# Kernel tuning notes

Measured on AMD Instinct MI355X. Metric: run time of the kernel, lower is better.

The kernel has to match this reference:

```python
import jax, jax.numpy as jnp
import numpy as np

B, S, T = 128, 1024, 512
VOCAB, E, HE, HD, ATT = 1000, 128, 64, 66, 32


def setup_inputs() -> dict:
    key = jax.random.key(0)
    ks = jax.random.split(key, 14)
    p = lambda k, shape: (jax.random.normal(k, shape, dtype=jnp.float32) * 0.05)
    return {
        'x': jax.random.randint(ks[0], (B, S), 0, VOCAB, dtype=jnp.int32),
        'c': jax.random.normal(ks[1], (B, T), dtype=jnp.float32),
        'emb': p(ks[2], (VOCAB, E)),
        'enc_Wih': p(ks[3], (4 * HE, E)),
        'enc_Whh': p(ks[4], (4 * HE, HE)),
        'enc_b': p(ks[5], (4 * HE,)),
        'att_fc_W': p(ks[6], (HE, E)),
        'att_fc_b': p(ks[7], (HE,)),
        'att_w_W': p(ks[8], (ATT, HE)),
        'att_w_b': p(ks[9], (ATT,)),
        'dec_Wih': p(ks[10], (4 * HD, ATT)),
        'dec_Whh': p(ks[11], (4 * HD, HD)),
        'dec_b': p(ks[12], (4 * HD,)),
        'fin_W': p(ks[13], (E, HD)),
        'fin_b': jnp.zeros((E,), dtype=jnp.float32),
    }


def _lstm_seq(xs, W_ih, W_hh, b, H):
    # xs: [B, S, in]; PyTorch gate order i, f, g, o
    bsz = xs.shape[0]
    gx = jnp.einsum('bsi,gi->bsg', xs, W_ih) + b  # [B,S,4H]

    def step(carry, g_t):
        h, c = carry
        g = g_t + h @ W_hh.T
        i, f, gg, o = jnp.split(g, 4, axis=-1)
        c = jax.nn.sigmoid(f) * c + jax.nn.sigmoid(i) * jnp.tanh(gg)
        h = jax.nn.sigmoid(o) * jnp.tanh(c)
        return (h, c), h

    h0 = jnp.zeros((bsz, H), xs.dtype)
    (_, _), hs = jax.lax.scan(step, (h0, h0), jnp.swapaxes(gx, 0, 1))
    return jnp.swapaxes(hs, 0, 1)  # [B,S,H]


def reference(x, c, emb, enc_Wih, enc_Whh, enc_b, att_fc_W, att_fc_b,
              att_w_W, att_w_b, dec_Wih, dec_Whh, dec_b, fin_W, fin_b):
    # encoder: embed + LSTM, returns full sequence of hidden states [B,S,64]
    enc = _lstm_seq(emb[x], enc_Wih, enc_Whh, enc_b, HE)
    bsz, steps = x.shape[0], c.shape[1]
    # initial decoder input: embedding of token 0, broadcast over batch
    x0 = jnp.broadcast_to(emb[0], (bsz, E))
    h0 = jnp.zeros((bsz, HD), enc.dtype)

    def step(carry, _):
        xemb, h, cc = carry
        # attend(a=xemb, A=enc)
        a = xemb @ att_fc_W.T + att_fc_b                     # [B,64]
        A = a[:, None, :] * enc                              # [B,S,64]
        alpha = jax.nn.softmax(
            jnp.tanh(jnp.einsum('bse,ae->bsa', A, att_w_W) + att_w_b),
            axis=-1)                                         # [B,S,32]
        beta = alpha.sum(axis=1)                             # [B,32]
        # decoder LSTM cell (one timestep)
        g = beta @ dec_Wih.T + h @ dec_Whh.T + dec_b
        i, f, gg, o = jnp.split(g, 4, axis=-1)
        cc = jax.nn.sigmoid(f) * cc + jax.nn.sigmoid(i) * jnp.tanh(gg)
        h = jax.nn.sigmoid(o) * jnp.tanh(cc)
        xemb = h @ fin_W.T + fin_b                           # feed back via final_fc
        return (xemb, h, cc), h

    _, hs = jax.lax.scan(step, (x0, h0, h0), None, length=steps)
    return jnp.swapaxes(hs, 0, 1)  # [B,T,66]
```

## Files before the change

kernel.cpp:

```cpp
#include <hip/hip_runtime.h>
#include <hip/hip_bf16.h>

#define kB 128
#define kS 1024
#define kT 512
#define kV 1000
#define kE 128
#define kHE 64
#define kHD 66
#define kATT 32
#define kGE 256
#define kGD 264

typedef __attribute__((ext_vector_type(4))) float f32x4;
typedef __attribute__((ext_vector_type(8))) short bf16x8;
typedef __attribute__((ext_vector_type(8))) unsigned short u16x8;

__device__ __forceinline__ unsigned short f2bf(float f) {
  unsigned int u = __builtin_bit_cast(unsigned int, f);
  u += 0x7FFFu + ((u >> 16) & 1u);
  return (unsigned short)(u >> 16);
}
__device__ __forceinline__ float rcp_(float x) { return __builtin_amdgcn_rcpf(x); }
__device__ __forceinline__ float fsig(float x)  { return rcp_(1.0f + __expf(-x)); }
__device__ __forceinline__ float ftanh(float x) { return 1.0f - 2.0f * rcp_(1.0f + __expf(2.0f * x)); }
__device__ __forceinline__ float fexp2(float z) {
#if __has_builtin(__builtin_amdgcn_exp2f)
  return __builtin_amdgcn_exp2f(z);
#else
  return __expf(z * 0.6931471805599453f);
#endif
}
__device__ __forceinline__ const unsigned short* launder_us(const unsigned short* p) {
  asm volatile("" : "+s"(p));
  return p;
}
__device__ __forceinline__ float dpp_red16(float v) {
  int x = __builtin_bit_cast(int, v);
  v += __builtin_bit_cast(float, __builtin_amdgcn_update_dpp(0, x, 0xB1, 0xf, 0xf, true));
  x = __builtin_bit_cast(int, v);
  v += __builtin_bit_cast(float, __builtin_amdgcn_update_dpp(0, x, 0x4E, 0xf, 0xf, true));
  x = __builtin_bit_cast(int, v);
  v += __builtin_bit_cast(float, __builtin_amdgcn_update_dpp(0, x, 0x124, 0xf, 0xf, true));
  x = __builtin_bit_cast(int, v);
  v += __builtin_bit_cast(float, __builtin_amdgcn_update_dpp(0, x, 0x128, 0xf, 0xf, true));
  return v;
}

__global__ __launch_bounds__(256) void prep_kernel(
    const float* __restrict__ emb, const float* __restrict__ enc_Wih,
    const float* __restrict__ enc_b, const float* __restrict__ enc_Whh,
    const float* __restrict__ att_fc_W, const float* __restrict__ att_fc_b,
    const float* __restrict__ att_w_W,
    const float* __restrict__ fin_W, const float* __restrict__ fin_b,
    const float* __restrict__ dec_Wih, const float* __restrict__ dec_Whh,
    const float* __restrict__ dec_b,
    float* __restrict__ embW, unsigned short* __restrict__ decF,
    unsigned short* __restrict__ encF, unsigned short* __restrict__ afF,
    float* __restrict__ wregF, float* __restrict__ dbias,
    float* __restrict__ wh64, float* __restrict__ wh65,
    float* __restrict__ abias, float* __restrict__ ainit) {
  int bid = blockIdx.x, tid = threadIdx.x;
  if (bid < kV) {
    float acc = enc_b[tid];
    const float* er = emb + bid * kE;
    const float* wr = enc_Wih + tid * kE;
    for (int e = 0; e < kE; ++e) acc += er[e] * wr[e];
    embW[bid * kGE + tid] = acc;
  } else if (bid == kV) {
    for (int i = tid; i < 17 * 3 * 64 * 8; i += 256) {
      int jj = i & 7, lane = (i >> 3) & 63, ts = i >> 9;
      int tile = ts / 3, ks = ts - tile * 3;
      int j = tile * 16 + (lane & 15);
      int k = ks * 32 + ((lane >> 4) << 3) + jj;
      float v = 0.f;
      if (j < kGD) {
        if (k < 32) v = dec_Wih[j * kATT + k];
        else v = dec_Whh[j * kHD + (k - 32)];
      }
      decF[i] = f2bf(v);
    }
  } else if (bid == kV + 1) {
    for (int i = tid; i < 16 * 2 * 64 * 8; i += 256) {
      int jj = i & 7, lane = (i >> 3) & 63, ts = i >> 9;
      int tile = ts >> 1, ks = ts & 1;
      int j = tile * 16 + (lane & 15);
      int k = ks * 32 + ((lane >> 4) << 3) + jj;
      encF[i] = f2bf(enc_Whh[j * kHE + k]);
    }
  } else if (bid == kV + 2) {
    for (int i = tid; i < 4 * 3 * 64 * 8; i += 256) {
      int jj = i & 7, lane = (i >> 3) & 63, ts = i >> 9;
      int tile = ts / 3, ks = ts - tile * 3;
      int aidx = tile * 16 + (lane & 15);
      int m = ks * 32 + ((lane >> 4) << 3) + jj;
      float v = 0.f;
      if (m < kHD)
        for (int e = 0; e < kE; ++e) v += att_fc_W[aidx * kE + e] * fin_W[e * kHD + m];
      afF[i] = f2bf(v);
    }
  } else if (bid == kV + 3) {
    for (int i = tid; i < 8 * 64 * 4; i += 256) {
      int c = i & 3, lane = (i >> 2) & 63, jq = i >> 8;
      int half = jq & 1, kc = (jq >> 1) & 1, mt = jq >> 2;
      wregF[i] = att_w_W[(mt * 16 + (lane & 15)) * kHE + kc * 32 + ((lane >> 4) << 3) + half * 4 + c];
    }
  } else if (bid == kV + 4) {
    for (int j = tid; j < kGD; j += 256) {
      float s = 0.f;
      for (int m = 0; m < kATT; ++m) s += dec_Wih[j * kATT + m];
      dbias[j] = dec_b[j] + 32.0f * s;
      wh64[j] = dec_Whh[j * kHD + 64];
      wh65[j] = dec_Whh[j * kHD + 65];
    }
  } else {
    if (tid < kHE) {
      float acc = att_fc_b[tid];
      for (int e = 0; e < kE; ++e) acc += att_fc_W[tid * kE + e] * fin_b[e];
      abias[tid] = acc;
    } else if (tid < 2 * kHE) {
      int a = tid - kHE;
      float acc = att_fc_b[a];
      for (int e = 0; e < kE; ++e) acc += emb[e] * att_fc_W[a * kE + e];
      ainit[a] = acc;
    }
  }
}

__global__ __launch_bounds__(256)
__attribute__((amdgpu_waves_per_eu(1, 1)))
void enc_kernel(
    const int* __restrict__ x, const float* __restrict__ embW,
    const unsigned short* __restrict__ encF, float* __restrict__ out) {
  __shared__ struct __align__(16) {
    unsigned short xe[64];
    float gbuf[kGE];
    int toks[kS];
  } sm;
  const int b = blockIdx.x, t = threadIdx.x, lane = t & 63, wv = t >> 6;

  for (int i = t; i < kS; i += 256) sm.toks[i] = x[b * kS + i];
  if (t < 64) sm.xe[t] = 0;

  u16x8 eQ[4][2];
  #pragma unroll
  for (int q = 0; q < 4; ++q)
    #pragma unroll
    for (int ks = 0; ks < 2; ++ks)
      eQ[q][ks] = *(const u16x8*)&encF[(((wv * 4 + q) * 2 + ks) * 64 + lane) * 8];
  __syncthreads();

  float gx0 = 0, gx1 = 0, gx2 = 0, gx3 = 0;
  if (lane < 16) {
    int tok = sm.toks[0];
    gx0 = embW[tok * kGE + wv * 64 + 0 + lane];
    gx1 = embW[tok * kGE + wv * 64 + 16 + lane];
    gx2 = embW[tok * kGE + wv * 64 + 32 + lane];
    gx3 = embW[tok * kGE + wv * 64 + 48 + lane];
  }
  float cE = 0.0f;
  unsigned short* eg = (unsigned short*)(out + (size_t)b * (kT * kHD));

  for (int s = 0; s < kS; ++s) {
    union { u16x8 u; bf16x8 v; } xa0, xa1;
    xa0.u = *(const u16x8*)&sm.xe[(lane >> 4) << 3];
    xa1.u = *(const u16x8*)&sm.xe[32 + ((lane >> 4) << 3)];
    float gn0 = 0, gn1 = 0, gn2 = 0, gn3 = 0;
    int tokn = sm.toks[(s + 1 < kS) ? (s + 1) : s];
    if (lane < 16) {
      gn0 = embW[tokn * kGE + wv * 64 + 0 + lane];
      gn1 = embW[tokn * kGE + wv * 64 + 16 + lane];
      gn2 = embW[tokn * kGE + wv * 64 + 32 + lane];
      gn3 = embW[tokn * kGE + wv * 64 + 48 + lane];
    }
    f32x4 z = {0.f, 0.f, 0.f, 0.f};
    f32x4 a0 = __builtin_amdgcn_mfma_f32_16x16x32_bf16(xa0.v, eQ[0][0], z, 0, 0, 0);
    a0 = __builtin_amdgcn_mfma_f32_16x16x32_bf16(xa1.v, eQ[0][1], a0, 0, 0, 0);
    f32x4 a1 = __builtin_amdgcn_mfma_f32_16x16x32_bf16(xa0.v, eQ[1][0], z, 0, 0, 0);
    a1 = __builtin_amdgcn_mfma_f32_16x16x32_bf16(xa1.v, eQ[1][1], a1, 0, 0, 0);
    f32x4 a2 = __builtin_amdgcn_mfma_f32_16x16x32_bf16(xa0.v, eQ[2][0], z, 0, 0, 0);
    a2 = __builtin_amdgcn_mfma_f32_16x16x32_bf16(xa1.v, eQ[2][1], a2, 0, 0, 0);
    f32x4 a3 = __builtin_amdgcn_mfma_f32_16x16x32_bf16(xa0.v, eQ[3][0], z, 0, 0, 0);
    a3 = __builtin_amdgcn_mfma_f32_16x16x32_bf16(xa1.v, eQ[3][1], a3, 0, 0, 0);
    if (lane < 16) {
      sm.gbuf[wv * 64 + 0 + lane]  = a0[0] + gx0;
      sm.gbuf[wv * 64 + 16 + lane] = a1[0] + gx1;
      sm.gbuf[wv * 64 + 32 + lane] = a2[0] + gx2;
      sm.gbuf[wv * 64 + 48 + lane] = a3[0] + gx3;
    }
    __syncthreads();
    if (t < 64) {
      float gi = sm.gbuf[t], gf = sm.gbuf[64 + t], gg = sm.gbuf[128 + t], go = sm.gbuf[192 + t];
      cE = fsig(gf) * cE + fsig(gi) * ftanh(gg);
      float h = fsig(go) * ftanh(cE);
      unsigned short hb = f2bf(h);
      sm.xe[t] = hb;
      eg[s * 64 + ((((t >> 3) ^ (s & 7)) << 3) | (t & 7))] = hb;
    }
    __syncthreads();
    gx0 = gn0; gx1 = gn1; gx2 = gn2; gx3 = gn3;
  }
}

struct __align__(16) DSm {
  unsigned short enc[kS * kHE];
  float wregL[8 * 64 * 4];
  unsigned short afL[4 * 3 * 64 * 8];
  float dbL[kGD];
  float wh64L[kGD];
  float wh65L[kGD];
  float absL[64];
  float aa[64];
  float beta[32];
  unsigned short xv[160];
  float gbuf[kGD];
  float hh2[2];
};

union U8 { u16x8 u; bf16x8 v; };

__global__ __launch_bounds__(512, 2)
void dec_kernel(
    const float* __restrict__ att_w_b,
    const unsigned short* __restrict__ decF, const unsigned short* __restrict__ afF,
    const float* __restrict__ wregF_ws, const float* __restrict__ dbias_ws,
    const float* __restrict__ wh64_ws, const float* __restrict__ wh65_ws,
    const float* __restrict__ abias_ws, const float* __restrict__ ainit_ws,
    float* __restrict__ out) {
  __shared__ DSm sm;
  const int b = blockIdx.x, t = threadIdx.x, lane = t & 63, wv = t >> 6;
  const int lr = lane & 15, g = lane >> 4;

  {
    const u16x8* src = (const u16x8*)(out + (size_t)b * (kT * kHD));
    u16x8* dst = (u16x8*)sm.enc;
    #pragma unroll
    for (int i = 0; i < 16; ++i) dst[t + i * 512] = src[t + i * 512];
  }
  ((f32x4*)sm.wregL)[t] = ((const f32x4*)wregF_ws)[t];
  for (int i = t; i < 768; i += 512) ((u16x8*)sm.afL)[i] = ((const u16x8*)afF)[i];
  for (int i = t; i < kGD; i += 512) {
    sm.dbL[i] = dbias_ws[i];
    sm.wh64L[i] = wh64_ws[i];
    sm.wh65L[i] = wh65_ws[i];
  }
  if (t < 64) { sm.absL[t] = abias_ws[t]; sm.aa[t] = ainit_ws[t]; }
  if (t < 32) sm.beta[t] = 0.f;
  if (t < 160) sm.xv[t] = 0;
  if (t < 2) sm.hh2[t] = 0.f;

  f32x4 wb0, wb1;
  #pragma unroll
  for (int r = 0; r < 4; ++r) {
    wb0[r] = att_w_b[g * 4 + r];
    wb1[r] = att_w_b[16 + g * 4 + r];
  }
  float cD = 0.0f, cD2 = 0.0f;
  __syncthreads();

  const int sbase = wv * 128;
  const int tileA = wv, tileB = wv + 8;
  const bool has3 = (wv == 7);

  for (int step = 0; step < kT; ++step) {
    U8 qa[3], qb[3], qc[3];
    {
      const f32x4* aap = (const f32x4*)sm.aa;
      const f32x4* wrl = (const f32x4*)sm.wregL;
      bf16x8 af[2][2];
      #pragma unroll
      for (int kc = 0; kc < 2; ++kc) {
        f32x4 a0v = aap[kc * 8 + g * 2];
        f32x4 a1v = aap[kc * 8 + g * 2 + 1];
        #pragma unroll
        for (int mt = 0; mt < 2; ++mt) {
          f32x4 w0 = wrl[((mt * 2 + kc) * 2 + 0) * 64 + lane];
          f32x4 w1 = wrl[((mt * 2 + kc) * 2 + 1) * 64 + lane];
          union { bf16x8 v; __hip_bfloat162 h2[4]; } tmp;
          tmp.h2[0] = __float22bfloat162_rn(make_float2(w0.x * a0v.x, w0.y * a0v.y));
          tmp.h2[1] = __float22bfloat162_rn(make_float2(w0.z * a0v.z, w0.w * a0v.w));
          tmp.h2[2] = __float22bfloat162_rn(make_float2(w1.x * a1v.x, w1.y * a1v.y));
          tmp.h2[3] = __float22bfloat162_rn(make_float2(w1.z * a1v.z, w1.w * a1v.w));
          af[mt][kc] = tmp.v;
        }
      }
      float betaAcc[2][4] = {};
      float amax = 0.0f;
      #pragma unroll
      for (int nt = 0; nt < 8; ++nt) {
        int s = sbase + nt * 16 + lr;
        int sw = s & 7;
        U8 e0, e1;
        e0.u = *(const u16x8*)&sm.enc[s * kHE + ((g ^ sw) << 3)];
        e1.u = *(const u16x8*)&sm.enc[s * kHE + (((4 + g) ^ sw) << 3)];
        f32x4 acc0 = __builtin_amdgcn_mfma_f32_16x16x32_bf16(af[0][0], e0.v, wb0, 0, 0, 0);
        acc0 = __builtin_amdgcn_mfma_f32_16x16x32_bf16(af[0][1], e1.v, acc0, 0, 0, 0);
        f32x4 acc1 = __builtin_amdgcn_mfma_f32_16x16x32_bf16(af[1][0], e0.v, wb1, 0, 0, 0);
        acc1 = __builtin_amdgcn_mfma_f32_16x16x32_bf16(af[1][1], e1.v, acc1, 0, 0, 0);
        float u0[4], u1[4], dsum = 0.f;
        #pragma unroll
        for (int r = 0; r < 4; ++r) {
          float x0 = acc0[r], x1 = acc1[r];
          amax = fmaxf(amax, fmaxf(__builtin_fabsf(x0), __builtin_fabsf(x1)));
          u0[r] = fexp2(x0 * __builtin_fmaf(x0 * x0, -0.48089835f, 1.44269504f));
          u1[r] = fexp2(x1 * __builtin_fmaf(x1 * x1, -0.48089835f, 1.44269504f));
          dsum += u0[r] + u1[r];
        }
        dsum += __shfl_xor(dsum, 16);
        dsum += __shfl_xor(dsum, 32);
        float invd = rcp_(dsum);
        #pragma unroll
        for (int r = 0; r < 4; ++r) {
          betaAcc[0][r] += u0[r] * invd;
          betaAcc[1][r] += u1[r] * invd;
        }
      }
      if (__builtin_expect(__any(amax > 0.35f), 0)) {
        #pragma unroll
        for (int mt = 0; mt < 2; ++mt)
          #pragma unroll
          for (int r = 0; r < 4; ++r) betaAcc[mt][r] = 0.f;
        for (int nt = 0; nt < 8; ++nt) {
          int s = sbase + nt * 16 + lr;
          int sw = s & 7;
          U8 e0, e1;
          e0.u = *(const u16x8*)&sm.enc[s * kHE + ((g ^ sw) << 3)];
          e1.u = *(const u16x8*)&sm.enc[s * kHE + (((4 + g) ^ sw) << 3)];
          f32x4 acc0 = __builtin_amdgcn_mfma_f32_16x16x32_bf16(af[0][0], e0.v, wb0, 0, 0, 0);
          acc0 = __builtin_amdgcn_mfma_f32_16x16x32_bf16(af[0][1], e1.v, acc0, 0, 0, 0);
          f32x4 acc1 = __builtin_amdgcn_mfma_f32_16x16x32_bf16(af[1][0], e0.v, wb1, 0, 0, 0);
          acc1 = __builtin_amdgcn_mfma_f32_16x16x32_bf16(af[1][1], e1.v, acc1, 0, 0, 0);
          float u0[4], u1[4], dsum = 0.f;
          for (int r = 0; r < 4; ++r) {
            u0[r] = __expf(tanhf(acc0[r]));
            u1[r] = __expf(tanhf(acc1[r]));
            dsum += u0[r] + u1[r];
          }
          dsum += __shfl_xor(dsum, 16);
          dsum += __shfl_xor(dsum, 32);
          float invd = rcp_(dsum);
          for (int r = 0; r < 4; ++r) {
            betaAcc[0][r] += u0[r] * invd;
            betaAcc[1][r] += u1[r] * invd;
          }
        }
      }
      {
        const unsigned short* dFp = launder_us(decF);
        #pragma unroll
        for (int ks = 0; ks < 3; ++ks) {
          qa[ks].u = *(const u16x8*)&dFp[((tileA * 3 + ks) * 64 + lane) * 8];
          qb[ks].u = *(const u16x8*)&dFp[((tileB * 3 + ks) * 64 + lane) * 8];
        }
        if (has3) {
          #pragma unroll
          for (int ks = 0; ks < 3; ++ks)
            qc[ks].u = *(const u16x8*)&dFp[((16 * 3 + ks) * 64 + lane) * 8];
        }
      }
      #pragma unroll
      for (int mt = 0; mt < 2; ++mt)
        #pragma unroll
        for (int r = 0; r < 4; ++r) {
          float v = dpp_red16(betaAcc[mt][r]);
          if (lr == 0) atomicAdd(&sm.beta[mt * 16 + g * 4 + r], v);
        }
    }
    __syncthreads();
    {
      const f32x4* pb = (const f32x4*)sm.beta;
      f32x4 b0 = pb[g * 2], b1 = pb[g * 2 + 1];
      union { bf16x8 v; __hip_bfloat162 h2[4]; } bfr;
      bfr.h2[0] = __float22bfloat162_rn(make_float2(b0.x - 32.f, b0.y - 32.f));
      bfr.h2[1] = __float22bfloat162_rn(make_float2(b0.z - 32.f, b0.w - 32.f));
      bfr.h2[2] = __float22bfloat162_rn(make_float2(b1.x - 32.f, b1.y - 32.f));
      bfr.h2[3] = __float22bfloat162_rn(make_float2(b1.z - 32.f, b1.w - 32.f));
      U8 xg1, xg2;
      xg1.u = *(const u16x8*)&sm.xv[32 + (g << 3)];
      xg2.u = *(const u16x8*)&sm.xv[64 + (g << 3)];
      float hh0 = sm.hh2[0], hh1 = sm.hh2[1];
      f32x4 z = {0.f, 0.f, 0.f, 0.f};
      f32x4 ga = __builtin_amdgcn_mfma_f32_16x16x32_bf16(bfr.v, qa[0].v, z, 0, 0, 0);
      ga = __builtin_amdgcn_mfma_f32_16x16x32_bf16(xg1.v, qa[1].v, ga, 0, 0, 0);
      ga = __builtin_amdgcn_mfma_f32_16x16x32_bf16(xg2.v, qa[2].v, ga, 0, 0, 0);
      f32x4 gb = __builtin_amdgcn_mfma_f32_16x16x32_bf16(bfr.v, qb[0].v, z, 0, 0, 0);
      gb = __builtin_amdgcn_mfma_f32_16x16x32_bf16(xg1.v, qb[1].v, gb, 0, 0, 0);
      gb = __builtin_amdgcn_mfma_f32_16x16x32_bf16(xg2.v, qb[2].v, gb, 0, 0, 0);
      if (lane < 16) {
        int ja = tileA * 16 + lane;
        sm.gbuf[ja] = ga[0] + sm.dbL[ja] + sm.wh64L[ja] * hh0 + sm.wh65L[ja] * hh1;
        int jb = tileB * 16 + lane;
        sm.gbuf[jb] = gb[0] + sm.dbL[jb] + sm.wh64L[jb] * hh0 + sm.wh65L[jb] * hh1;
      }
      if (has3) {
        f32x4 gc = __builtin_amdgcn_mfma_f32_16x16x32_bf16(bfr.v, qc[0].v, z, 0, 0, 0);
        gc = __builtin_amdgcn_mfma_f32_16x16x32_bf16(xg1.v, qc[1].v, gc, 0, 0, 0);
        gc = __builtin_amdgcn_mfma_f32_16x16x32_bf16(xg2.v, qc[2].v, gc, 0, 0, 0);
        if (lane < 8) {
          int jc = 256 + lane;
          sm.gbuf[jc] = gc[0] + sm.dbL[jc] + sm.wh64L[jc] * hh0 + sm.wh65L[jc] * hh1;
        }
      }
    }
    __syncthreads();
    if (wv == 0) {
      float gi = sm.gbuf[lane], gf = sm.gbuf[66 + lane], gg = sm.gbuf[132 + lane], go = sm.gbuf[198 + lane];
      cD = fsig(gf) * cD + fsig(gi) * ftanh(gg);
      float h = fsig(go) * ftanh(cD);
      sm.xv[32 + lane] = f2bf(h);
      out[((size_t)b * kT + step) * kHD + lane] = h;
      if (lane < 2) {
        float gi2 = sm.gbuf[64 + lane], gf2 = sm.gbuf[130 + lane], gg2 = sm.gbuf[196 + lane], go2 = sm.gbuf[262 + lane];
        cD2 = fsig(gf2) * cD2 + fsig(gi2) * ftanh(gg2);
        float h2 = fsig(go2) * ftanh(cD2);
        sm.xv[96 + lane] = f2bf(h2);
        sm.hh2[lane] = h2;
        out[((size_t)b * kT + step) * kHD + 64 + lane] = h2;
      }
      U8 y0, y1, y2;
      y0.u = *(const u16x8*)&sm.xv[32 + (g << 3)];
      y1.u = *(const u16x8*)&sm.xv[64 + (g << 3)];
      y2.u = *(const u16x8*)&sm.xv[96 + (g << 3)];
      f32x4 z = {0.f, 0.f, 0.f, 0.f};
      #pragma unroll
      for (int tt = 0; tt < 4; ++tt) {
        U8 f0, f1, f2;
        f0.u = *(const u16x8*)&sm.afL[((tt * 3 + 0) * 64 + lane) * 8];
        f1.u = *(const u16x8*)&sm.afL[((tt * 3 + 1) * 64 + lane) * 8];
        f2.u = *(const u16x8*)&sm.afL[((tt * 3 + 2) * 64 + lane) * 8];
        f32x4 acc = __builtin_amdgcn_mfma_f32_16x16x32_bf16(y0.v, f0.v, z, 0, 0, 0);
        acc = __builtin_amdgcn_mfma_f32_16x16x32_bf16(y1.v, f1.v, acc, 0, 0, 0);
        acc = __builtin_amdgcn_mfma_f32_16x16x32_bf16(y2.v, f2.v, acc, 0, 0, 0);
        if (lane < 16) sm.aa[tt * 16 + lane] = acc[0] + sm.absL[tt * 16 + lane];
      }
      if (lane < 32) sm.beta[lane] = 0.f;
    }
    __syncthreads();
  }
}

extern "C" void kernel_launch(void* const* d_in, const int* in_sizes, int n_in,
                              void* d_out, int out_size, void* d_ws, size_t ws_size,
                              hipStream_t stream) {
  const int*   x        = (const int*)d_in[0];
  const float* emb      = (const float*)d_in[2];
  const float* enc_Wih  = (const float*)d_in[3];
  const float* enc_Whh  = (const float*)d_in[4];
  const float* enc_b    = (const float*)d_in[5];
  const float* att_fc_W = (const float*)d_in[6];
  const float* att_fc_b = (const float*)d_in[7];
  const float* att_w_W  = (const float*)d_in[8];
  const float* att_w_b  = (const float*)d_in[9];
  const float* dec_Wih  = (const float*)d_in[10];
  const float* dec_Whh  = (const float*)d_in[11];
  const float* dec_b    = (const float*)d_in[12];
  const float* fin_W    = (const float*)d_in[13];
  const float* fin_b    = (const float*)d_in[14];
  float* out = (float*)d_out;

  float* embW = (float*)d_ws;
  unsigned short* decF = (unsigned short*)(embW + kV * kGE);
  unsigned short* encF = decF + 17 * 3 * 64 * 8;
  unsigned short* afF  = encF + 16 * 2 * 64 * 8;
  float* wregF = (float*)(afF + 4 * 3 * 64 * 8);
  float* dbias = wregF + 8 * 64 * 4;
  float* wh64  = dbias + kGD;
  float* wh65  = wh64 + kGD;
  float* abias = wh65 + kGD;
  float* ainit = abias + kHE;

  prep_kernel<<<dim3(kV + 6), dim3(256), 0, stream>>>(
      emb, enc_Wih, enc_b, enc_Whh, att_fc_W, att_fc_b, att_w_W, fin_W, fin_b,
      dec_Wih, dec_Whh, dec_b, embW, decF, encF, afF, wregF, dbias, wh64, wh65,
      abias, ainit);
  enc_kernel<<<dim3(kB), dim3(256), 0, stream>>>(x, embW, encF, out);
  dec_kernel<<<dim3(kB), dim3(512), 0, stream>>>(
      att_w_b, decF, afF, wregF, dbias, wh64, wh65, abias, ainit, out);
}
```

Measured before the change: 2.867 ms.

## Run decoder with 1024 threads per block, halving per-wave sequence work

The decoder block grows from 8 to 16 waves. Each wave now handles 64 sequence positions instead of 128 and one gate tile instead of two, with the last wave also computing the remaining tail tile. This shortens the serial per-step critical path of the 512-step recurrence, at the cost of more threads contending at each barrier and fewer registers per thread. The tanh approximation gains a cubic term and the fallback threshold is raised from 0.35 to 0.6, so the exact fallback path is taken less often at some accuracy risk.

```diff
diff --git a/kernel.cpp b/kernel.cpp
--- a/kernel.cpp
+++ b/kernel.cpp
@@ -210,6 +210,7 @@
   float wh64L[kGD];
   float wh65L[kGD];
   float absL[64];
+  float wbL[32];
   float aa[64];
   float beta[32];
   unsigned short xv[160];
@@ -219,7 +220,7 @@
 
 union U8 { u16x8 u; bf16x8 v; };
 
-__global__ __launch_bounds__(512, 2)
+__global__ __launch_bounds__(1024)
 void dec_kernel(
     const float* __restrict__ att_w_b,
     const unsigned short* __restrict__ decF, const unsigned short* __restrict__ afF,
@@ -235,38 +236,34 @@
     const u16x8* src = (const u16x8*)(out + (size_t)b * (kT * kHD));
     u16x8* dst = (u16x8*)sm.enc;
     #pragma unroll
-    for (int i = 0; i < 16; ++i) dst[t + i * 512] = src[t + i * 512];
-  }
-  ((f32x4*)sm.wregL)[t] = ((const f32x4*)wregF_ws)[t];
-  for (int i = t; i < 768; i += 512) ((u16x8*)sm.afL)[i] = ((const u16x8*)afF)[i];
-  for (int i = t; i < kGD; i += 512) {
+    for (int i = 0; i < 8; ++i) dst[t + i * 1024] = src[t + i * 1024];
+  }
+  if (t < 512) ((f32x4*)sm.wregL)[t] = ((const f32x4*)wregF_ws)[t];
+  if (t < 768) ((u16x8*)sm.afL)[t] = ((const u16x8*)afF)[t];
+  for (int i = t; i < kGD; i += 1024) {
     sm.dbL[i] = dbias_ws[i];
     sm.wh64L[i] = wh64_ws[i];
     sm.wh65L[i] = wh65_ws[i];
   }
   if (t < 64) { sm.absL[t] = abias_ws[t]; sm.aa[t] = ainit_ws[t]; }
-  if (t < 32) sm.beta[t] = 0.f;
+  if (t < 32) { sm.beta[t] = 0.f; sm.wbL[t] = att_w_b[t]; }
   if (t < 160) sm.xv[t] = 0;
   if (t < 2) sm.hh2[t] = 0.f;
 
-  f32x4 wb0, wb1;
-  #pragma unroll
-  for (int r = 0; r < 4; ++r) {
-    wb0[r] = att_w_b[g * 4 + r];
-    wb1[r] = att_w_b[16 + g * 4 + r];
-  }
   float cD = 0.0f, cD2 = 0.0f;
   __syncthreads();
 
-  const int sbase = wv * 128;
-  const int tileA = wv, tileB = wv + 8;
-  const bool has3 = (wv == 7);
+  const int sbase = wv * 64;
+  const int tileA = wv;
+  const bool has2 = (wv == 15);
 
   for (int step = 0; step < kT; ++step) {
-    U8 qa[3], qb[3], qc[3];
+    U8 qa[3];
     {
       const f32x4* aap = (const f32x4*)sm.aa;
       const f32x4* wrl = (const f32x4*)sm.wregL;
+      const f32x4* wbp = (const f32x4*)sm.wbL;
+      f32x4 wb0 = wbp[g], wb1 = wbp[4 + g];
       bf16x8 af[2][2];
       #pragma unroll
       for (int kc = 0; kc < 2; ++kc) {
@@ -287,7 +284,7 @@
       float betaAcc[2][4] = {};
       float amax = 0.0f;
       #pragma unroll
-      for (int nt = 0; nt < 8; ++nt) {
+      for (int nt = 0; nt < 4; ++nt) {
         int s = sbase + nt * 16 + lr;
         int sw = s & 7;
         U8 e0, e1;
@@ -302,8 +299,9 @@
         for (int r = 0; r < 4; ++r) {
           float x0 = acc0[r], x1 = acc1[r];
           amax = fmaxf(amax, fmaxf(__builtin_fabsf(x0), __builtin_fabsf(x1)));
-          u0[r] = fexp2(x0 * __builtin_fmaf(x0 * x0, -0.48089835f, 1.44269504f));
-          u1[r] = fexp2(x1 * __builtin_fmaf(x1 * x1, -0.48089835f, 1.44269504f));
+          float t0 = x0 * x0, t1 = x1 * x1;
+          u0[r] = fexp2(x0 * __builtin_fmaf(t0, __builtin_fmaf(t0, 0.19235935f, -0.48089835f), 1.44269504f));
+          u1[r] = fexp2(x1 * __builtin_fmaf(t1, __builtin_fmaf(t1, 0.19235935f, -0.48089835f), 1.44269504f));
           dsum += u0[r] + u1[r];
         }
         dsum += __shfl_xor(dsum, 16);
@@ -315,12 +313,12 @@
           betaAcc[1][r] += u1[r] * invd;
         }
       }
-      if (__builtin_expect(__any(amax > 0.35f), 0)) {
+      if (__builtin_expect(__any(amax > 0.6f), 0)) {
         #pragma unroll
         for (int mt = 0; mt < 2; ++mt)
           #pragma unroll
           for (int r = 0; r < 4; ++r) betaAcc[mt][r] = 0.f;
-        for (int nt = 0; nt < 8; ++nt) {
+        for (int nt = 0; nt < 4; ++nt) {
           int s = sbase + nt * 16 + lr;
           int sw = s & 7;
           U8 e0, e1;
@@ -348,15 +346,8 @@
       {
         const unsigned short* dFp = launder_us(decF);
         #pragma unroll
-        for (int ks = 0; ks < 3; ++ks) {
+        for (int ks = 0; ks < 3; ++ks)
           qa[ks].u = *(const u16x8*)&dFp[((tileA * 3 + ks) * 64 + lane) * 8];
-          qb[ks].u = *(const u16x8*)&dFp[((tileB * 3 + ks) * 64 + lane) * 8];
-        }
-        if (has3) {
-          #pragma unroll
-          for (int ks = 0; ks < 3; ++ks)
-            qc[ks].u = *(const u16x8*)&dFp[((16 * 3 + ks) * 64 + lane) * 8];
-        }
       }
       #pragma unroll
       for (int mt = 0; mt < 2; ++mt)
@@ -368,6 +359,13 @@
     }
     __syncthreads();
     {
+      U8 qc[3];
+      if (has2) {
+        const unsigned short* dFp = launder_us(decF);
+        #pragma unroll
+        for (int ks = 0; ks < 3; ++ks)
+          qc[ks].u = *(const u16x8*)&dFp[((16 * 3 + ks) * 64 + lane) * 8];
+      }
       const f32x4* pb = (const f32x4*)sm.beta;
       f32x4 b0 = pb[g * 2], b1 = pb[g * 2 + 1];
       union { bf16x8 v; __hip_bfloat162 h2[4]; } bfr;
@@ -383,16 +381,11 @@
       f32x4 ga = __builtin_amdgcn_mfma_f32_16x16x32_bf16(bfr.v, qa[0].v, z, 0, 0, 0);
       ga = __builtin_amdgcn_mfma_f32_16x16x32_bf16(xg1.v, qa[1].v, ga, 0, 0, 0);
       ga = __builtin_amdgcn_mfma_f32_16x16x32_bf16(xg2.v, qa[2].v, ga, 0, 0, 0);
-      f32x4 gb = __builtin_amdgcn_mfma_f32_16x16x32_bf16(bfr.v, qb[0].v, z, 0, 0, 0);
-      gb = __builtin_amdgcn_mfma_f32_16x16x32_bf16(xg1.v, qb[1].v, gb, 0, 0, 0);
-      gb = __builtin_amdgcn_mfma_f32_16x16x32_bf16(xg2.v, qb[2].v, gb, 0, 0, 0);
       if (lane < 16) {
         int ja = tileA * 16 + lane;
         sm.gbuf[ja] = ga[0] + sm.dbL[ja] + sm.wh64L[ja] * hh0 + sm.wh65L[ja] * hh1;
-        int jb = tileB * 16 + lane;
-        sm.gbuf[jb] = gb[0] + sm.dbL[jb] + sm.wh64L[jb] * hh0 + sm.wh65L[jb] * hh1;
-      }
-      if (has3) {
+      }
+      if (has2) {
         f32x4 gc = __builtin_amdgcn_mfma_f32_16x16x32_bf16(bfr.v, qc[0].v, z, 0, 0, 0);
         gc = __builtin_amdgcn_mfma_f32_16x16x32_bf16(xg1.v, qc[1].v, gc, 0, 0, 0);
         gc = __builtin_amdgcn_mfma_f32_16x16x32_bf16(xg2.v, qc[2].v, gc, 0, 0, 0);
@@ -474,6 +467,6 @@
       dec_Wih, dec_Whh, dec_b, embW, decF, encF, afF, wregF, dbias, wh64, wh65,
       abias, ainit);
   enc_kernel<<<dim3(kB), dim3(256), 0, stream>>>(x, embW, encF, out);
-  dec_kernel<<<dim3(kB), dim3(512), 0, stream>>>(
+  dec_kernel<<<dim3(kB), dim3(1024), 0, stream>>>(
       att_w_b, decF, afF, wregF, dbias, wh64, wh65, abias, ainit, out);
 }
```

Result: slower. 3.374 ms (+17.7%).

## Interleave decoder gate columns and fuse LSTM cell update into gate MFMA waves

Applied to the files above, without the earlier changes.

Permutes decoder gate weight columns so each cell's four gates land in adjacent lanes. Every wave can then compute the LSTM cell update in registers right after its gate MFMA, with DPP quad broadcasts and tanh computed through sigmoid. This removes the gbuf shared-memory round trip and the serial wave-0 cell update. The h state buffer is double-buffered so the update can write the next step's input without racing readers. It adds redundant sigmoid work across lanes and more complex indexing.

```diff
diff --git a/kernel.cpp b/kernel.cpp
--- a/kernel.cpp
+++ b/kernel.cpp
@@ -46,6 +46,7 @@
   v += __builtin_bit_cast(float, __builtin_amdgcn_update_dpp(0, x, 0x128, 0xf, 0xf, true));
   return v;
 }
+#define DPPB(v, ctrl) __builtin_bit_cast(float, __builtin_amdgcn_update_dpp(0, __builtin_bit_cast(int, (v)), (ctrl), 0xf, 0xf, true))
 
 __global__ __launch_bounds__(256) void prep_kernel(
     const float* __restrict__ emb, const float* __restrict__ enc_Wih,
@@ -71,10 +72,12 @@
     for (int i = tid; i < 17 * 3 * 64 * 8; i += 256) {
       int jj = i & 7, lane = (i >> 3) & 63, ts = i >> 9;
       int tile = ts / 3, ks = ts - tile * 3;
-      int j = tile * 16 + (lane & 15);
+      int jp = tile * 16 + (lane & 15);
+      int cell = jp >> 2, gate = jp & 3;
       int k = ks * 32 + ((lane >> 4) << 3) + jj;
       float v = 0.f;
-      if (j < kGD) {
+      if (cell < kHD) {
+        int j = gate * kHD + cell;
         if (k < 32) v = dec_Wih[j * kATT + k];
         else v = dec_Whh[j * kHD + (k - 32)];
       }
@@ -106,12 +109,14 @@
       wregF[i] = att_w_W[(mt * 16 + (lane & 15)) * kHE + kc * 32 + ((lane >> 4) << 3) + half * 4 + c];
     }
   } else if (bid == kV + 4) {
-    for (int j = tid; j < kGD; j += 256) {
+    for (int jp = tid; jp < kGD; jp += 256) {
+      int cell = jp >> 2, gate = jp & 3;
+      int j = gate * kHD + cell;
       float s = 0.f;
       for (int m = 0; m < kATT; ++m) s += dec_Wih[j * kATT + m];
-      dbias[j] = dec_b[j] + 32.0f * s;
-      wh64[j] = dec_Whh[j * kHD + 64];
-      wh65[j] = dec_Whh[j * kHD + 65];
+      dbias[jp] = dec_b[j] + 32.0f * s;
+      wh64[jp] = dec_Whh[j * kHD + 64];
+      wh65[jp] = dec_Whh[j * kHD + 65];
     }
   } else {
     if (tid < kHE) {
@@ -212,9 +217,8 @@
   float absL[64];
   float aa[64];
   float beta[32];
-  unsigned short xv[160];
-  float gbuf[kGD];
-  float hh2[2];
+  unsigned short xv[2][160];
+  float hh2[2][2];
 };
 
 union U8 { u16x8 u; bf16x8 v; };
@@ -246,8 +250,8 @@
   }
   if (t < 64) { sm.absL[t] = abias_ws[t]; sm.aa[t] = ainit_ws[t]; }
   if (t < 32) sm.beta[t] = 0.f;
-  if (t < 160) sm.xv[t] = 0;
-  if (t < 2) sm.hh2[t] = 0.f;
+  for (int i = t; i < 320; i += 512) ((unsigned short*)sm.xv)[i] = 0;
+  if (t < 4) ((float*)sm.hh2)[t] = 0.f;
 
   f32x4 wb0, wb1;
   #pragma unroll
@@ -255,7 +259,7 @@
     wb0[r] = att_w_b[g * 4 + r];
     wb1[r] = att_w_b[16 + g * 4 + r];
   }
-  float cD = 0.0f, cD2 = 0.0f;
+  float cDa = 0.0f, cDb = 0.0f, cDc = 0.0f;
   __syncthreads();
 
   const int sbase = wv * 128;
@@ -263,6 +267,7 @@
   const bool has3 = (wv == 7);
 
   for (int step = 0; step < kT; ++step) {
+    const int cb = step & 1, nb = cb ^ 1;
     U8 qa[3], qb[3], qc[3];
     {
       const f32x4* aap = (const f32x4*)sm.aa;
@@ -376,51 +381,75 @@
       bfr.h2[2] = __float22bfloat162_rn(make_float2(b1.x - 32.f, b1.y - 32.f));
       bfr.h2[3] = __float22bfloat162_rn(make_float2(b1.z - 32.f, b1.w - 32.f));
       U8 xg1, xg2;
-      xg1.u = *(const u16x8*)&sm.xv[32 + (g << 3)];
-      xg2.u = *(const u16x8*)&sm.xv[64 + (g << 3)];
-      float hh0 = sm.hh2[0], hh1 = sm.hh2[1];
+      xg1.u = *(const u16x8*)&sm.xv[cb][32 + (g << 3)];
+      xg2.u = *(const u16x8*)&sm.xv[cb][64 + (g << 3)];
+      float hh0 = sm.hh2[cb][0], hh1 = sm.hh2[cb][1];
+      float* op = out + ((size_t)b * kT + step) * kHD;
+      const int gate = lane & 3;
+      const float kk = (gate == 2) ? 2.0f : 1.0f;
       f32x4 z = {0.f, 0.f, 0.f, 0.f};
-      f32x4 ga = __builtin_amdgcn_mfma_f32_16x16x32_bf16(bfr.v, qa[0].v, z, 0, 0, 0);
-      ga = __builtin_amdgcn_mfma_f32_16x16x32_bf16(xg1.v, qa[1].v, ga, 0, 0, 0);
-      ga = __builtin_amdgcn_mfma_f32_16x16x32_bf16(xg2.v, qa[2].v, ga, 0, 0, 0);
-      f32x4 gb = __builtin_amdgcn_mfma_f32_16x16x32_bf16(bfr.v, qb[0].v, z, 0, 0, 0);
-      gb = __builtin_amdgcn_mfma_f32_16x16x32_bf16(xg1.v, qb[1].v, gb, 0, 0, 0);
-      gb = __builtin_amdgcn_mfma_f32_16x16x32_bf16(xg2.v, qb[2].v, gb, 0, 0, 0);
-      if (lane < 16) {
-        int ja = tileA * 16 + lane;
-        sm.gbuf[ja] = ga[0] + sm.dbL[ja] + sm.wh64L[ja] * hh0 + sm.wh65L[ja] * hh1;
-        int jb = tileB * 16 + lane;
-        sm.gbuf[jb] = gb[0] + sm.dbL[jb] + sm.wh64L[jb] * hh0 + sm.wh65L[jb] * hh1;
+      {
+        f32x4 ga = __builtin_amdgcn_mfma_f32_16x16x32_bf16(bfr.v, qa[0].v, z, 0, 0, 0);
+        ga = __builtin_amdgcn_mfma_f32_16x16x32_bf16(xg1.v, qa[1].v, ga, 0, 0, 0);
+        ga = __builtin_amdgcn_mfma_f32_16x16x32_bf16(xg2.v, qa[2].v, ga, 0, 0, 0);
+        int jp = tileA * 16 + lr;
+        float xg = ga[0] + sm.dbL[jp] + sm.wh64L[jp] * hh0 + sm.wh65L[jp] * hh1;
+        float y = fsig(kk * xg);
+        float v = (gate == 2) ? (2.0f * y - 1.0f) : y;
+        float q0 = DPPB(v, 0x00), q1 = DPPB(v, 0x55), q2 = DPPB(v, 0xAA), q3 = DPPB(v, 0xFF);
+        float cn = q1 * cDa + q0 * q2;
+        cDa = cn;
+        float h = q3 * ftanh(cn);
+        if (gate == 0 && lane < 16) {
+          int cell = jp >> 2;
+          sm.xv[nb][32 + cell] = f2bf(h);
+          op[cell] = h;
+        }
+      }
+      {
+        f32x4 gb = __builtin_amdgcn_mfma_f32_16x16x32_bf16(bfr.v, qb[0].v, z, 0, 0, 0);
+        gb = __builtin_amdgcn_mfma_f32_16x16x32_bf16(xg1.v, qb[1].v, gb, 0, 0, 0);
+        gb = __builtin_amdgcn_mfma_f32_16x16x32_bf16(xg2.v, qb[2].v, gb, 0, 0, 0);
+        int jp = tileB * 16 + lr;
+        float xg = gb[0] + sm.dbL[jp] + sm.wh64L[jp] * hh0 + sm.wh65L[jp] * hh1;
+        float y = fsig(kk * xg);
+        float v = (gate == 2) ? (2.0f * y - 1.0f) : y;
+        float q0 = DPPB(v, 0x00), q1 = DPPB(v, 0x55), q2 = DPPB(v, 0xAA), q3 = DPPB(v, 0xFF);
+        float cn = q1 * cDb + q0 * q2;
+        cDb = cn;
+        float h = q3 * ftanh(cn);
+        if (gate == 0 && lane < 16) {
+          int cell = jp >> 2;
+          sm.xv[nb][32 + cell] = f2bf(h);
+          op[cell] = h;
+        }
       }
       if (has3) {
         f32x4 gc = __builtin_amdgcn_mfma_f32_16x16x32_bf16(bfr.v, qc[0].v, z, 0, 0, 0);
         gc = __builtin_amdgcn_mfma_f32_16x16x32_bf16(xg1.v, qc[1].v, gc, 0, 0, 0);
         gc = __builtin_amdgcn_mfma_f32_16x16x32_bf16(xg2.v, qc[2].v, gc, 0, 0, 0);
-        if (lane < 8) {
-          int jc = 256 + lane;
-          sm.gbuf[jc] = gc[0] + sm.dbL[jc] + sm.wh64L[jc] * hh0 + sm.wh65L[jc] * hh1;
+        int jp = 256 + (lane & 7);
+        float xg = gc[0] + sm.dbL[jp] + sm.wh64L[jp] * hh0 + sm.wh65L[jp] * hh1;
+        float y = fsig(kk * xg);
+        float v = (gate == 2) ? (2.0f * y - 1.0f) : y;
+        float q0 = DPPB(v, 0x00), q1 = DPPB(v, 0x55), q2 = DPPB(v, 0xAA), q3 = DPPB(v, 0xFF);
+        float cn = q1 * cDc + q0 * q2;
+        cDc = cn;
+        float h = q3 * ftanh(cn);
+        if (gate == 0 && lane < 8) {
+          int cell = 64 + (lane >> 2);
+          sm.xv[nb][32 + cell] = f2bf(h);
+          sm.hh2[nb][lane >> 2] = h;
+          op[cell] = h;
         }
       }
     }
     __syncthreads();
     if (wv == 0) {
-      float gi = sm.gbuf[lane], gf = sm.gbuf[66 + lane], gg = sm.gbuf[132 + lane], go = sm.gbuf[198 + lane];
-      cD = fsig(gf) * cD + fsig(gi) * ftanh(gg);
-      float h = fsig(go) * ftanh(cD);
-      sm.xv[32 + lane] = f2bf(h);
-      out[((size_t)b * kT + step) * kHD + lane] = h;
-      if (lane < 2) {
-        float gi2 = sm.gbuf[64 + lane], gf2 = sm.gbuf[130 + lane], gg2 = sm.gbuf[196 + lane], go2 = sm.gbuf[262 + lane];
-        cD2 = fsig(gf2) * cD2 + fsig(gi2) * ftanh(gg2);
-        float h2 = fsig(go2) * ftanh(cD2);
-        sm.xv[96 + lane] = f2bf(h2);
-        sm.hh2[lane] = h2;
-        out[((size_t)b * kT + step) * kHD + 64 + lane] = h2;
-      }
       U8 y0, y1, y2;
-      y0.u = *(const u16x8*)&sm.xv[32 + (g << 3)];
-      y1.u = *(const u16x8*)&sm.xv[64 + (g << 3)];
-      y2.u = *(const u16x8*)&sm.xv[96 + (g << 3)];
+      y0.u = *(const u16x8*)&sm.xv[nb][32 + (g << 3)];
+      y1.u = *(const u16x8*)&sm.xv[nb][64 + (g << 3)];
+      y2.u = *(const u16x8*)&sm.xv[nb][96 + (g << 3)];
       f32x4 z = {0.f, 0.f, 0.f, 0.f};
       #pragma unroll
       for (int tt = 0; tt < 4; ++tt) {
```

New measurement: 2.823 ms. About the same (-1.5%).
